# Kernel optimization log

Hardware: AMD Instinct MI355X
Metric: run time of the kernel (lower is better)

## Reference

```python
import jax, jax.numpy as jnp
import numpy as np

DIM = 512
HEADS = 8
EPS = 1e-3  # keras LayerNormalization default epsilon


def setup_inputs() -> dict:
    key = jax.random.key(0)
    ks = jax.random.split(key, 12)
    B, H, W, C = 8, 32, 32, DIM
    s = 0.02
    return {
        "x": jax.random.normal(ks[0], (B, H, W, C), jnp.float32),
        "ln_gamma": jnp.ones((C,), jnp.float32),
        "ln_beta": jnp.zeros((C,), jnp.float32),
        "qkv_d_w": jax.random.normal(ks[1], (C, 3 * C), jnp.float32) * s,
        "qkv_d_b": jnp.zeros((3 * C,), jnp.float32),
        "qkv_s_w": jax.random.normal(ks[2], (C, 3 * C), jnp.float32) * s,
        "qkv_s_b": jnp.zeros((3 * C,), jnp.float32),
        "proj_d_w": jax.random.normal(ks[3], (C, C), jnp.float32) * s,
        "proj_d_b": jnp.zeros((C,), jnp.float32),
        "proj_s_w": jax.random.normal(ks[4], (C, C), jnp.float32) * s,
        "proj_s_b": jnp.zeros((C,), jnp.float32),
        "fusion_weight": jnp.ones((2,), jnp.float32),
    }


def _split_heads(t, B, N):
    # [B, N, C] -> [B, heads, N, head_dim]
    return t.reshape(B, N, HEADS, -1).transpose(0, 2, 1, 3)


def _merge_heads(t, B, N, C):
    # [B, heads, N, head_dim] -> [B, N, C]
    return t.transpose(0, 2, 1, 3).reshape(B, N, C)


def reference(x, ln_gamma, ln_beta, qkv_d_w, qkv_d_b, qkv_s_w, qkv_s_b,
              proj_d_w, proj_d_b, proj_s_w, proj_s_b, fusion_weight):
    B, H, W, C = x.shape
    N = H * W
    scale = (C // HEADS) ** -0.5

    xf = x.reshape(B, N, C)
    mu = jnp.mean(xf, axis=-1, keepdims=True)
    var = jnp.var(xf, axis=-1, keepdims=True)
    xf = (xf - mu) * jax.lax.rsqrt(var + EPS) * ln_gamma + ln_beta

    # dense (softmax) branch
    qkv_d = xf @ qkv_d_w + qkv_d_b
    q_d, k_d, v_d = (
        _split_heads(t, B, N) for t in jnp.split(qkv_d, 3, axis=-1)
    )
    logits_d = jnp.einsum("bhnd,bhmd->bhnm", q_d, k_d) * scale
    out_d = jnp.einsum("bhnm,bhmd->bhnd", jax.nn.softmax(logits_d, axis=-1), v_d)
    out_d = _merge_heads(out_d, B, N, C) @ proj_d_w + proj_d_b

    # sparse (relu^2) branch
    qkv_s = xf @ qkv_s_w + qkv_s_b
    q_s, k_s, v_s = (
        _split_heads(t, B, N) for t in jnp.split(qkv_s, 3, axis=-1)
    )
    rq = jnp.square(jax.nn.relu(q_s))
    rk = jnp.square(jax.nn.relu(k_s))
    logits_s = jnp.einsum("bhnd,bhmd->bhnm", rq, rk) * scale
    out_s = jnp.einsum("bhnm,bhmd->bhnd", logits_s, v_s)
    out_s = _merge_heads(out_s, B, N, C) @ proj_s_w + proj_s_b

    alpha = jax.nn.softmax(fusion_weight)
    out = alpha[0] * out_s + alpha[1] * out_d
    return out.reshape(B, H, W, C)
```

## Files before the change

kernel.cpp:

```cpp
#include <hip/hip_runtime.h>
#include <math.h>

#define M_ROWS   8192
#define CDIM     512
#define QKV_N    1536
#define NTOK     1024
#define HEADS    8
#define HD       64
#define EPS      1e-3f
#define SCALE    0.125f
#define SCL2E    0.18033688011112042f

typedef __attribute__((ext_vector_type(8))) short short8;
typedef __attribute__((ext_vector_type(4))) float f32x4;
typedef unsigned short ushort_t;


__device__ __forceinline__ ushort_t f2bf(float f) {
    union { float f; unsigned int u; } v; v.f = f;
    unsigned int r = v.u + 0x7fffu + ((v.u >> 16) & 1u);
    return (ushort_t)(r >> 16);
}
__device__ __forceinline__ float bf2f(ushort_t u) {
    union { unsigned int u; float f; } v; v.u = ((unsigned int)u) << 16;
    return v.f;
}

__device__ __forceinline__ void get_alpha(const float* __restrict__ fw,
                                          float& a0, float& a1)
{
    const float m  = fmaxf(fw[0], fw[1]);
    const float e0 = __expf(fw[0] - m);
    const float e1 = __expf(fw[1] - m);
    const float inv = 1.0f / (e0 + e1);
    a0 = e0 * inv;
    a1 = e1 * inv;
}


__global__ __launch_bounds__(256) void ln_kernel(const float* __restrict__ x,
                                                 const float* __restrict__ gamma,
                                                 const float* __restrict__ beta,
                                                 ushort_t* __restrict__ xhi,
                                                 ushort_t* __restrict__ xlo)
{
    const int row = blockIdx.x;
    const int t   = threadIdx.x;
    const float2 v = ((const float2*)(x + (size_t)row * CDIM))[t];
    float s  = v.x + v.y;
    float ss = v.x * v.x + v.y * v.y;
#pragma unroll
    for (int off = 32; off > 0; off >>= 1) {
        s  += __shfl_xor(s,  off, 64);
        ss += __shfl_xor(ss, off, 64);
    }
    __shared__ float red[8];
    __shared__ float stats[2];
    const int wid = t >> 6, lane = t & 63;
    if (lane == 0) { red[wid] = s; red[4 + wid] = ss; }
    __syncthreads();
    if (t == 0) {
        const float S  = red[0] + red[1] + red[2] + red[3];
        const float SS = red[4] + red[5] + red[6] + red[7];
        const float mu  = S * (1.0f / CDIM);
        const float var = SS * (1.0f / CDIM) - mu * mu;
        stats[0] = mu;
        stats[1] = rsqrtf(var + EPS);
    }
    __syncthreads();
    const float mu = stats[0], rs = stats[1];
    const float2 gv = ((const float2*)gamma)[t];
    const float2 bv = ((const float2*)beta)[t];
    const float ox = (v.x - mu) * rs * gv.x + bv.x;
    const float oy = (v.y - mu) * rs * gv.y + bv.y;
    ushort2 h2, l2;
    h2.x = f2bf(ox); l2.x = f2bf(ox - bf2f(h2.x));
    h2.y = f2bf(oy); l2.y = f2bf(oy - bf2f(h2.y));
    ((ushort2*)(xhi + (size_t)row * CDIM))[t] = h2;
    ((ushort2*)(xlo + (size_t)row * CDIM))[t] = l2;
}


__global__ __launch_bounds__(256) void tconv_kernel(const float* __restrict__ W,
                                                    ushort_t* __restrict__ hiT,
                                                    ushort_t* __restrict__ loT,
                                                    int N, int ors, int coff)
{
    const int t  = threadIdx.x;
    const int bk = blockIdx.x * 64, bn = blockIdx.y * 64;
    __shared__ float tile[64][65];
#pragma unroll
    for (int i = 0; i < 4; ++i) {
        const int idx = t + i * 256;
        const int kl = idx >> 4, nl = (idx & 15) * 4;
        const float4 v = *(const float4*)(W + (size_t)(bk + kl) * N + bn + nl);
        tile[kl][nl] = v.x; tile[kl][nl + 1] = v.y;
        tile[kl][nl + 2] = v.z; tile[kl][nl + 3] = v.w;
    }
    __syncthreads();
#pragma unroll
    for (int i = 0; i < 2; ++i) {
        const int idx = t + i * 256;
        const int nl = idx >> 3, kc = (idx & 7) * 8;
        short8 hv, lv;
#pragma unroll
        for (int j = 0; j < 8; ++j) {
            const float f = tile[kc + j][nl];
            const ushort_t h = f2bf(f);
            hv[j] = (short)h;
            lv[j] = (short)f2bf(f - bf2f(h));
        }
        const size_t ob = (size_t)(bn + nl) * ors + coff + bk + kc;
        *(short8*)(hiT + ob) = hv;
        if (loT) *(short8*)(loT + ob) = lv;
    }
}


template<int MODE, int OUTBF>
__global__ __launch_bounds__(256) void gemm_bf16_mfma(const ushort_t* __restrict__ Ahi,
                                                      const ushort_t* __restrict__ Alo,
                                                      const ushort_t* __restrict__ Bhi,
                                                      const ushort_t* __restrict__ Blo,
                                                      const float* __restrict__ bias,
                                                      float* __restrict__ C,
                                                      ushort_t* __restrict__ Cb,
                                                      int N, int K)
{
    const int t  = threadIdx.x;
    const int l  = t & 63, w = t >> 6;
    const int wr = w >> 1, wc = w & 1;
    const int lr = l & 15, lg = l >> 4;
    const int bm = blockIdx.x * 128, bn = blockIdx.y * 128;

    __shared__ ushort_t As[MODE ? 2 : 1][128 * 64];
    __shared__ ushort_t Bs[MODE ? 2 : 1][128 * 64];

    f32x4 acc[4][4];
#pragma unroll
    for (int i = 0; i < 4; ++i)
#pragma unroll
        for (int j = 0; j < 4; ++j) acc[i][j] = (f32x4){0.f, 0.f, 0.f, 0.f};

    const int srow0  = t >> 3;
    const int schunk = t & 7;

    for (int kt = 0; kt < K; kt += 64) {
        __syncthreads();
#pragma unroll
        for (int i = 0; i < 4; ++i) {
            const int row = srow0 + i * 32;
            const int cs  = ((schunk ^ (row & 7)) * 8);
            const size_t ga = (size_t)(bm + row) * K + kt + schunk * 8;
            const size_t gb = (size_t)(bn + row) * K + kt + schunk * 8;
            *(short8*)(&As[0][row * 64 + cs]) = *(const short8*)(Ahi + ga);
            *(short8*)(&Bs[0][row * 64 + cs]) = *(const short8*)(Bhi + gb);
            if (MODE) {
                *(short8*)(&As[MODE ? 1 : 0][row * 64 + cs]) = *(const short8*)(Alo + ga);
                *(short8*)(&Bs[MODE ? 1 : 0][row * 64 + cs]) = *(const short8*)(Blo + gb);
            }
        }
        __syncthreads();
#pragma unroll
        for (int ks = 0; ks < 2; ++ks) {
            short8 ah[4], bh[4], al[4], bl[4];
#pragma unroll
            for (int mf = 0; mf < 4; ++mf) {
                const int row = wr * 64 + mf * 16 + lr;
                const int cs  = (((ks * 4 + lg) ^ (row & 7)) * 8);
                ah[mf] = *(const short8*)(&As[0][row * 64 + cs]);
                if (MODE) al[mf] = *(const short8*)(&As[MODE ? 1 : 0][row * 64 + cs]);
            }
#pragma unroll
            for (int nf = 0; nf < 4; ++nf) {
                const int row = wc * 64 + nf * 16 + lr;
                const int cs  = (((ks * 4 + lg) ^ (row & 7)) * 8);
                bh[nf] = *(const short8*)(&Bs[0][row * 64 + cs]);
                if (MODE) bl[nf] = *(const short8*)(&Bs[MODE ? 1 : 0][row * 64 + cs]);
            }
#pragma unroll
            for (int mf = 0; mf < 4; ++mf)
#pragma unroll
                for (int nf = 0; nf < 4; ++nf) {
                    acc[mf][nf] = __builtin_amdgcn_mfma_f32_16x16x32_bf16(ah[mf], bh[nf], acc[mf][nf], 0, 0, 0);
                    if (MODE) {
                        acc[mf][nf] = __builtin_amdgcn_mfma_f32_16x16x32_bf16(al[mf], bh[nf], acc[mf][nf], 0, 0, 0);
                        acc[mf][nf] = __builtin_amdgcn_mfma_f32_16x16x32_bf16(ah[mf], bl[nf], acc[mf][nf], 0, 0, 0);
                    }
                }
        }
    }
    float bv[4];
#pragma unroll
    for (int nf = 0; nf < 4; ++nf) bv[nf] = bias[bn + wc * 64 + nf * 16 + lr];
#pragma unroll
    for (int mf = 0; mf < 4; ++mf)
#pragma unroll
        for (int r = 0; r < 4; ++r) {
            const int row = bm + wr * 64 + mf * 16 + lg * 4 + r;
            if (OUTBF) {
                ushort_t* cp = Cb + (size_t)row * N + bn + wc * 64;
#pragma unroll
                for (int nf = 0; nf < 4; ++nf)
                    cp[nf * 16 + lr] = f2bf(acc[mf][nf][r] + bv[nf]);
            } else {
                float* cp = C + (size_t)row * N + bn + wc * 64;
#pragma unroll
                for (int nf = 0; nf < 4; ++nf)
                    cp[nf * 16 + lr] = acc[mf][nf][r] + bv[nf];
            }
        }
}


__global__ __launch_bounds__(256) void gemm_proj(const ushort_t* __restrict__ Ahi,
                                                 const ushort_t* __restrict__ Alo,
                                                 const ushort_t* __restrict__ Bhi,
                                                 const ushort_t* __restrict__ Blo,
                                                 const float* __restrict__ bias,
                                                 float* __restrict__ C)
{
    const int t  = threadIdx.x;
    const int l  = t & 63, w = t >> 6;
    const int wr = w >> 1, wc = w & 1;
    const int lr = l & 15, lg = l >> 4;
    const int bm = blockIdx.x * 64, bn = blockIdx.y * 128;

    __shared__ ushort_t As[2][64 * 64];
    __shared__ ushort_t Bs[2][128 * 64];

    f32x4 acc[2][4];
#pragma unroll
    for (int i = 0; i < 2; ++i)
#pragma unroll
        for (int j = 0; j < 4; ++j) acc[i][j] = (f32x4){0.f, 0.f, 0.f, 0.f};

    const int srow0  = t >> 3;
    const int schunk = t & 7;

    for (int kt = 0; kt < 512; kt += 64) {
        __syncthreads();
#pragma unroll
        for (int i = 0; i < 2; ++i) {
            const int row = srow0 + i * 32;
            const int cs  = ((schunk ^ (row & 7)) * 8);
            const size_t ga = (size_t)(bm + row) * 1024 + kt + schunk * 8;
            *(short8*)(&As[0][row * 64 + cs]) = *(const short8*)(Ahi + ga);
            *(short8*)(&As[1][row * 64 + cs]) = *(const short8*)(Alo + ga);
        }
#pragma unroll
        for (int i = 0; i < 4; ++i) {
            const int row = srow0 + i * 32;
            const int cs  = ((schunk ^ (row & 7)) * 8);
            const size_t gb = (size_t)(bn + row) * 1024 + kt + schunk * 8;
            *(short8*)(&Bs[0][row * 64 + cs]) = *(const short8*)(Bhi + gb);
            *(short8*)(&Bs[1][row * 64 + cs]) = *(const short8*)(Blo + gb);
        }
        __syncthreads();
#pragma unroll
        for (int ks = 0; ks < 2; ++ks) {
            short8 ah[2], al[2], bh[4], bl[4];
#pragma unroll
            for (int mf = 0; mf < 2; ++mf) {
                const int row = wr * 32 + mf * 16 + lr;
                const int cs  = (((ks * 4 + lg) ^ (row & 7)) * 8);
                ah[mf] = *(const short8*)(&As[0][row * 64 + cs]);
                al[mf] = *(const short8*)(&As[1][row * 64 + cs]);
            }
#pragma unroll
            for (int nf = 0; nf < 4; ++nf) {
                const int row = wc * 64 + nf * 16 + lr;
                const int cs  = (((ks * 4 + lg) ^ (row & 7)) * 8);
                bh[nf] = *(const short8*)(&Bs[0][row * 64 + cs]);
                bl[nf] = *(const short8*)(&Bs[1][row * 64 + cs]);
            }
#pragma unroll
            for (int mf = 0; mf < 2; ++mf)
#pragma unroll
                for (int nf = 0; nf < 4; ++nf) {
                    acc[mf][nf] = __builtin_amdgcn_mfma_f32_16x16x32_bf16(ah[mf], bh[nf], acc[mf][nf], 0, 0, 0);
                    acc[mf][nf] = __builtin_amdgcn_mfma_f32_16x16x32_bf16(al[mf], bh[nf], acc[mf][nf], 0, 0, 0);
                    acc[mf][nf] = __builtin_amdgcn_mfma_f32_16x16x32_bf16(ah[mf], bl[nf], acc[mf][nf], 0, 0, 0);
                }
        }
    }

    for (int kt = 512; kt < 1024; kt += 64) {
        __syncthreads();
#pragma unroll
        for (int i = 0; i < 2; ++i) {
            const int row = srow0 + i * 32;
            const int cs  = ((schunk ^ (row & 7)) * 8);
            const size_t ga = (size_t)(bm + row) * 1024 + kt + schunk * 8;
            *(short8*)(&As[0][row * 64 + cs]) = *(const short8*)(Ahi + ga);
        }
#pragma unroll
        for (int i = 0; i < 4; ++i) {
            const int row = srow0 + i * 32;
            const int cs  = ((schunk ^ (row & 7)) * 8);
            const size_t gb = (size_t)(bn + row) * 1024 + kt + schunk * 8;
            *(short8*)(&Bs[0][row * 64 + cs]) = *(const short8*)(Bhi + gb);
        }
        __syncthreads();
#pragma unroll
        for (int ks = 0; ks < 2; ++ks) {
            short8 ah[2], bh[4];
#pragma unroll
            for (int mf = 0; mf < 2; ++mf) {
                const int row = wr * 32 + mf * 16 + lr;
                const int cs  = (((ks * 4 + lg) ^ (row & 7)) * 8);
                ah[mf] = *(const short8*)(&As[0][row * 64 + cs]);
            }
#pragma unroll
            for (int nf = 0; nf < 4; ++nf) {
                const int row = wc * 64 + nf * 16 + lr;
                const int cs  = (((ks * 4 + lg) ^ (row & 7)) * 8);
                bh[nf] = *(const short8*)(&Bs[0][row * 64 + cs]);
            }
#pragma unroll
            for (int mf = 0; mf < 2; ++mf)
#pragma unroll
                for (int nf = 0; nf < 4; ++nf)
                    acc[mf][nf] = __builtin_amdgcn_mfma_f32_16x16x32_bf16(ah[mf], bh[nf], acc[mf][nf], 0, 0, 0);
        }
    }

    float bv[4];
#pragma unroll
    for (int nf = 0; nf < 4; ++nf) bv[nf] = bias[bn + wc * 64 + nf * 16 + lr];
#pragma unroll
    for (int mf = 0; mf < 2; ++mf)
#pragma unroll
        for (int r = 0; r < 4; ++r) {
            const int row = bm + wr * 32 + mf * 16 + lg * 4 + r;
            float* cp = C + (size_t)row * CDIM + bn + wc * 64;
#pragma unroll
            for (int nf = 0; nf < 4; ++nf)
                cp[nf * 16 + lr] = acc[mf][nf][r] + bv[nf];
        }
}


__global__ __launch_bounds__(256) void vt_kernel(const ushort_t* __restrict__ qkvd_bf,
                                                 ushort_t* __restrict__ vtg)
{
    const int t  = threadIdx.x;
    const int bh = blockIdx.x, nt = blockIdx.y;
    const int b  = bh >> 3, h = bh & 7;
    __shared__ ushort_t tile[64 * 72];
    const int row = t >> 2, c16 = (t & 3) * 16;
    const size_t src = (size_t)(b * NTOK + nt * 64 + row) * QKV_N + 2 * CDIM + h * HD + c16;
    *(short8*)(tile + row * 72 + c16)     = *(const short8*)(qkvd_bf + src);
    *(short8*)(tile + row * 72 + c16 + 8) = *(const short8*)(qkvd_bf + src + 8);
    __syncthreads();
    const int d = t >> 2, tc = (t & 3) * 16;
    short8 o0, o1;
#pragma unroll
    for (int i = 0; i < 8; ++i) {
        o0[i] = (short)tile[(tc + i) * 72 + d];
        o1[i] = (short)tile[(tc + 8 + i) * 72 + d];
    }
    const size_t dst = ((size_t)bh * 64 + d) * NTOK + nt * 64 + tc;
    *(short8*)(vtg + dst)     = o0;
    *(short8*)(vtg + dst + 8) = o1;
}


__global__ __launch_bounds__(256) void attn_dense_mfma(const ushort_t* __restrict__ qkvd_bf,
                                                       const ushort_t* __restrict__ vtg,
                                                       const float* __restrict__ fw,
                                                       ushort_t* __restrict__ athi)
{
    const int t  = threadIdx.x;
    const int l  = t & 63;
    const int w  = t >> 6;
    const int lr = l & 15;
    const int lg = l >> 4;

    const int blk = blockIdx.x;
    const int xcd = blk & 7;
    const int ixl = blk >> 3;
    const int bh  = ((ixl >> 4) << 3) + xcd;
    const int qt  = ixl & 15;
    const int b   = bh >> 3, h = bh & 7;

    __shared__ ushort_t Qs[64 * 72];
    __shared__ ushort_t Ks[64 * 72];
    __shared__ ushort_t Vs[64 * 72];
    __shared__ ushort_t Pq[64 * 72];

    const int srow = t >> 2, sc = (t & 3) * 16;

    {
        const size_t src = (size_t)(b * NTOK + qt * 64 + srow) * QKV_N + h * HD + sc;
        *(short8*)(Qs + srow * 72 + sc)     = *(const short8*)(qkvd_bf + src);
        *(short8*)(Qs + srow * 72 + sc + 8) = *(const short8*)(qkvd_bf + src + 8);
    }
    __syncthreads();

    const short8 bQ0 = *(const short8*)(Qs + (w * 16 + lr) * 72 + lg * 8);
    const short8 bQ1 = *(const short8*)(Qs + (w * 16 + lr) * 72 + 32 + lg * 8);

    f32x4 oacc[4];
#pragma unroll
    for (int i = 0; i < 4; ++i) oacc[i] = (f32x4){0.f, 0.f, 0.f, 0.f};
    float lsum = 0.f;

    for (int kt2 = 0; kt2 < 16; ++kt2) {
        __syncthreads();
        {
            const size_t ksrc = (size_t)(b * NTOK + kt2 * 64 + srow) * QKV_N + CDIM + h * HD + sc;
            *(short8*)(Ks + srow * 72 + sc)     = *(const short8*)(qkvd_bf + ksrc);
            *(short8*)(Ks + srow * 72 + sc + 8) = *(const short8*)(qkvd_bf + ksrc + 8);
            const size_t vsrc = ((size_t)bh * 64 + srow) * NTOK + kt2 * 64 + sc;
            *(short8*)(Vs + srow * 72 + sc)     = *(const short8*)(vtg + vsrc);
            *(short8*)(Vs + srow * 72 + sc + 8) = *(const short8*)(vtg + vsrc + 8);
        }
        __syncthreads();

#pragma unroll
        for (int kb = 0; kb < 4; ++kb) {
            const short8 aK0 = *(const short8*)(Ks + (kb * 16 + lr) * 72 + lg * 8);
            const short8 aK1 = *(const short8*)(Ks + (kb * 16 + lr) * 72 + 32 + lg * 8);
            f32x4 z = {0.f, 0.f, 0.f, 0.f};
            z = __builtin_amdgcn_mfma_f32_16x16x32_bf16(aK0, bQ0, z, 0, 0, 0);
            z = __builtin_amdgcn_mfma_f32_16x16x32_bf16(aK1, bQ1, z, 0, 0, 0);
            const float p0 = exp2f(z[0] * SCL2E);
            const float p1 = exp2f(z[1] * SCL2E);
            const float p2 = exp2f(z[2] * SCL2E);
            const float p3 = exp2f(z[3] * SCL2E);
            lsum += (p0 + p1) + (p2 + p3);
            unsigned int r01, r23;
            asm("v_cvt_pk_bf16_f32 %0, %1, %2" : "=v"(r01) : "v"(p0), "v"(p1));
            asm("v_cvt_pk_bf16_f32 %0, %1, %2" : "=v"(r23) : "v"(p2), "v"(p3));
            uint2 pw; pw.x = r01; pw.y = r23;
            *(uint2*)(Pq + (w * 16 + lr) * 72 + kb * 16 + lg * 4) = pw;
        }

        const short8 bP0 = *(const short8*)(Pq + (w * 16 + lr) * 72 + lg * 8);
        const short8 bP1 = *(const short8*)(Pq + (w * 16 + lr) * 72 + 32 + lg * 8);
#pragma unroll
        for (int nfd = 0; nfd < 4; ++nfd) {
            const short8 aV0 = *(const short8*)(Vs + (nfd * 16 + lr) * 72 + lg * 8);
            const short8 aV1 = *(const short8*)(Vs + (nfd * 16 + lr) * 72 + 32 + lg * 8);
            oacc[nfd] = __builtin_amdgcn_mfma_f32_16x16x32_bf16(aV0, bP0, oacc[nfd], 0, 0, 0);
            oacc[nfd] = __builtin_amdgcn_mfma_f32_16x16x32_bf16(aV1, bP1, oacc[nfd], 0, 0, 0);
        }
    }

    lsum += __shfl_xor(lsum, 16, 64);
    lsum += __shfl_xor(lsum, 32, 64);
    float a0, a1;
    get_alpha(fw, a0, a1);
    const float sc2 = a1 / lsum;
    const size_t orow = ((size_t)(b * NTOK + qt * 64 + w * 16 + lr)) * 1024 + CDIM + h * HD;
#pragma unroll
    for (int nfd = 0; nfd < 4; ++nfd) {
        ushort4 hw;
#pragma unroll
        for (int r = 0; r < 4; ++r)
            ((ushort_t*)&hw)[r] = f2bf(oacc[nfd][r] * sc2);
        *(ushort4*)(athi + orow + nfd * 16 + lg * 4) = hw;
    }
}


__global__ __launch_bounds__(256) void sparse_kv_kernel(const float* __restrict__ qkvs,
                                                        float* __restrict__ kvpart)
{
    const int t     = threadIdx.x;
    const int bh    = blockIdx.x >> 2;
    const int chunk = blockIdx.x & 3;
    const int b     = bh >> 3, h = bh & 7;
    const int j     = t >> 2, g = t & 3;
    __shared__ __align__(16) float ks[64 * 68];
    __shared__ __align__(16) float vs[64 * 68];
    float4 acc[4];
#pragma unroll
    for (int c4 = 0; c4 < 4; ++c4) acc[c4] = make_float4(0.f, 0.f, 0.f, 0.f);

    const size_t bbase = (size_t)b * NTOK * QKV_N;
    for (int mt = chunk * 4; mt < chunk * 4 + 4; ++mt) {
        __syncthreads();
        {
            const float* ksrc = qkvs + bbase + (size_t)(mt * 64) * QKV_N + CDIM + h * HD;
            const float* vsrc = ksrc + CDIM;
#pragma unroll
            for (int i = 0; i < 4; ++i) {
                const int idx = t + i * 256;
                const int row = idx >> 4, c4 = (idx & 15) * 4;
                *(float4*)(ks + row * 68 + c4) = *(const float4*)(ksrc + (size_t)row * QKV_N + c4);
                *(float4*)(vs + row * 68 + c4) = *(const float4*)(vsrc + (size_t)row * QKV_N + c4);
            }
        }
        __syncthreads();
#pragma unroll 4
        for (int m = 0; m < 64; ++m) {
            const float kkv = ks[m * 68 + j];
            const float rk  = fmaxf(kkv, 0.f);
            const float rk2 = rk * rk;
#pragma unroll
            for (int c4 = 0; c4 < 4; ++c4) {
                const float4 vv = *(const float4*)(vs + m * 68 + g * 16 + c4 * 4);
                acc[c4].x += rk2 * vv.x; acc[c4].y += rk2 * vv.y;
                acc[c4].z += rk2 * vv.z; acc[c4].w += rk2 * vv.w;
            }
        }
    }
#pragma unroll
    for (int c4 = 0; c4 < 4; ++c4) {
        float4 w = acc[c4];
        w.x *= SCALE; w.y *= SCALE; w.z *= SCALE; w.w *= SCALE;
        *(float4*)(kvpart + ((size_t)blockIdx.x << 12) + j * 64 + g * 16 + c4 * 4) = w;
    }
}


__global__ __launch_bounds__(256) void sparse_out_kernel(const float* __restrict__ qkvs,
                                                         const float* __restrict__ kvpart,
                                                         const float* __restrict__ fw,
                                                         ushort_t* __restrict__ athi,
                                                         ushort_t* __restrict__ atlo)
{
    const int t   = threadIdx.x;
    const int blk = blockIdx.x;
    const int qt  = blk & 15;
    const int bh  = blk >> 4;
    const int b   = bh >> 3, h = bh & 7;
    const int r   = t >> 2, g = t & 3;
    __shared__ __align__(16) float qs[64 * 68];
    __shared__ __align__(16) float kvs[64 * 68];
    {
        const float* qsrc = qkvs + (size_t)b * NTOK * QKV_N + (size_t)(qt * 64) * QKV_N + h * HD;
        const float* p0 = kvpart + ((size_t)(bh * 4) << 12);
#pragma unroll
        for (int i = 0; i < 4; ++i) {
            const int idx = t + i * 256;
            const int row = idx >> 4, c4 = (idx & 15) * 4;
            *(float4*)(qs + row * 68 + c4) = *(const float4*)(qsrc + (size_t)row * QKV_N + c4);
            const int o = row * 64 + c4;
            float4 s0 = *(const float4*)(p0 + o);
            const float4 s1 = *(const float4*)(p0 + 4096 + o);
            const float4 s2 = *(const float4*)(p0 + 8192 + o);
            const float4 s3 = *(const float4*)(p0 + 12288 + o);
            s0.x += s1.x + s2.x + s3.x; s0.y += s1.y + s2.y + s3.y;
            s0.z += s1.z + s2.z + s3.z; s0.w += s1.w + s2.w + s3.w;
            *(float4*)(kvs + row * 68 + c4) = s0;
        }
    }
    __syncthreads();
    float4 acc[4];
#pragma unroll
    for (int c4 = 0; c4 < 4; ++c4) acc[c4] = make_float4(0.f, 0.f, 0.f, 0.f);
#pragma unroll 4
    for (int jj = 0; jj < 64; ++jj) {
        const float qv  = qs[r * 68 + jj];
        const float rq  = fmaxf(qv, 0.f);
        const float rq2 = rq * rq;
#pragma unroll
        for (int c4 = 0; c4 < 4; ++c4) {
            const float4 kvv = *(const float4*)(kvs + jj * 68 + g * 16 + c4 * 4);
            acc[c4].x += rq2 * kvv.x; acc[c4].y += rq2 * kvv.y;
            acc[c4].z += rq2 * kvv.z; acc[c4].w += rq2 * kvv.w;
        }
    }
    float a0, a1;
    get_alpha(fw, a0, a1);
    const size_t orow = ((size_t)(b * NTOK + qt * 64 + r)) * 1024 + h * HD;
#pragma unroll
    for (int c4 = 0; c4 < 4; ++c4) {
        float4 w = acc[c4];
        w.x *= a0; w.y *= a0; w.z *= a0; w.w *= a0;
        ushort4 hw, lw;
        hw.x = f2bf(w.x); lw.x = f2bf(w.x - bf2f(hw.x));
        hw.y = f2bf(w.y); lw.y = f2bf(w.y - bf2f(hw.y));
        hw.z = f2bf(w.z); lw.z = f2bf(w.z - bf2f(hw.z));
        hw.w = f2bf(w.w); lw.w = f2bf(w.w - bf2f(hw.w));
        *(ushort4*)(athi + orow + g * 16 + c4 * 4) = hw;
        *(ushort4*)(atlo + orow + g * 16 + c4 * 4) = lw;
    }
}


__global__ void bias_comb_kernel(const float* __restrict__ bs,
                                 const float* __restrict__ bd,
                                 const float* __restrict__ fw,
                                 float* __restrict__ out)
{
    float a0, a1;
    get_alpha(fw, a0, a1);
    const int t = threadIdx.x;
    out[t] = a0 * bs[t] + a1 * bd[t];
}


extern "C" void kernel_launch(void* const* d_in, const int* in_sizes, int n_in,
                              void* d_out, int out_size, void* d_ws, size_t ws_size,
                              hipStream_t stream)
{
    (void)in_sizes; (void)n_in; (void)out_size; (void)ws_size;

    const float* x        = (const float*)d_in[0];
    const float* ln_g     = (const float*)d_in[1];
    const float* ln_b     = (const float*)d_in[2];
    const float* qkv_d_w  = (const float*)d_in[3];
    const float* qkv_d_b  = (const float*)d_in[4];
    const float* qkv_s_w  = (const float*)d_in[5];
    const float* qkv_s_b  = (const float*)d_in[6];
    const float* proj_d_w = (const float*)d_in[7];
    const float* proj_d_b = (const float*)d_in[8];
    const float* proj_s_w = (const float*)d_in[9];
    const float* proj_s_b = (const float*)d_in[10];
    const float* fw       = (const float*)d_in[11];

    float* ws = (float*)d_ws;
    float*    qkvs    = ws;
    float*    kvpart  = ws + (size_t)12582912;
    float*    biasc   = ws + (size_t)13631488;
    ushort_t* qkvd_bf = (ushort_t*)(ws + (size_t)14680064);
    ushort_t* vtg     = (ushort_t*)(ws + (size_t)20971520);
    ushort_t* athi    = (ushort_t*)(ws + (size_t)23068672);
    ushort_t* atlo    = (ushort_t*)(ws + (size_t)27262976);
    ushort_t* xhi     = (ushort_t*)(ws + (size_t)31457280);
    ushort_t* xlo     = (ushort_t*)(ws + (size_t)33554432);
    ushort_t* WdT_hi  = (ushort_t*)(ws + (size_t)35651584);
    ushort_t* WsT_hi  = (ushort_t*)(ws + (size_t)36044800);
    ushort_t* WsT_lo  = (ushort_t*)(ws + (size_t)36438016);
    ushort_t* WpT_hi  = (ushort_t*)(ws + (size_t)36831232);
    ushort_t* WpT_lo  = (ushort_t*)(ws + (size_t)37093376);

    ln_kernel<<<8192, 256, 0, stream>>>(x, ln_g, ln_b, xhi, xlo);
    tconv_kernel<<<dim3(8, 24), 256, 0, stream>>>(qkv_d_w, WdT_hi, nullptr, QKV_N, CDIM, 0);
    tconv_kernel<<<dim3(8, 24), 256, 0, stream>>>(qkv_s_w, WsT_hi, WsT_lo, QKV_N, CDIM, 0);
    tconv_kernel<<<dim3(8, 8), 256, 0, stream>>>(proj_s_w, WpT_hi, WpT_lo, CDIM, 1024, 0);
    tconv_kernel<<<dim3(8, 8), 256, 0, stream>>>(proj_d_w, WpT_hi, nullptr, CDIM, 1024, 512);
    bias_comb_kernel<<<1, 512, 0, stream>>>(proj_s_b, proj_d_b, fw, biasc);

    gemm_bf16_mfma<0, 1><<<dim3(64, 12), 256, 0, stream>>>(xhi, nullptr, WdT_hi, nullptr,
                                                           qkv_d_b, nullptr, qkvd_bf,
                                                           QKV_N, CDIM);
    gemm_bf16_mfma<1, 0><<<dim3(64, 12), 256, 0, stream>>>(xhi, xlo, WsT_hi, WsT_lo,
                                                           qkv_s_b, qkvs, nullptr,
                                                           QKV_N, CDIM);

    vt_kernel<<<dim3(64, 16), 256, 0, stream>>>(qkvd_bf, vtg);
    attn_dense_mfma<<<1024, 256, 0, stream>>>(qkvd_bf, vtg, fw, athi);

    sparse_kv_kernel<<<256, 256, 0, stream>>>(qkvs, kvpart);
    sparse_out_kernel<<<1024, 256, 0, stream>>>(qkvs, kvpart, fw, athi, atlo);

    gemm_proj<<<dim3(128, 4), 256, 0, stream>>>(athi, atlo, WpT_hi, WpT_lo,
                                                biasc, (float*)d_out);
}
```

Measured before the change: 198.6 us.

## Merge independent kernels into combined launches and add MFMA priority hints

Merges the layernorm, four weight-transpose conversions and the bias combine into one prep kernel that branches on block index. It likewise pairs the V-transpose with the sparse KV reduction, and the dense attention with the sparse output stage, so independent work shares a launch. This cuts launch count and the idle gaps between small kernels, and lets the two attention branches overlap on the GPU. It also wraps the attention MFMA sections in s_setprio. The cost is larger shared memory per block, since each merged kernel reserves the bigger branch's buffer, which may lower occupancy.

```diff
diff --git a/kernel.cpp b/kernel.cpp
--- a/kernel.cpp
+++ b/kernel.cpp
@@ -38,57 +38,13 @@
 }
 
 
-__global__ __launch_bounds__(256) void ln_kernel(const float* __restrict__ x,
-                                                 const float* __restrict__ gamma,
-                                                 const float* __restrict__ beta,
-                                                 ushort_t* __restrict__ xhi,
-                                                 ushort_t* __restrict__ xlo)
-{
-    const int row = blockIdx.x;
-    const int t   = threadIdx.x;
-    const float2 v = ((const float2*)(x + (size_t)row * CDIM))[t];
-    float s  = v.x + v.y;
-    float ss = v.x * v.x + v.y * v.y;
-#pragma unroll
-    for (int off = 32; off > 0; off >>= 1) {
-        s  += __shfl_xor(s,  off, 64);
-        ss += __shfl_xor(ss, off, 64);
-    }
-    __shared__ float red[8];
-    __shared__ float stats[2];
-    const int wid = t >> 6, lane = t & 63;
-    if (lane == 0) { red[wid] = s; red[4 + wid] = ss; }
-    __syncthreads();
-    if (t == 0) {
-        const float S  = red[0] + red[1] + red[2] + red[3];
-        const float SS = red[4] + red[5] + red[6] + red[7];
-        const float mu  = S * (1.0f / CDIM);
-        const float var = SS * (1.0f / CDIM) - mu * mu;
-        stats[0] = mu;
-        stats[1] = rsqrtf(var + EPS);
-    }
-    __syncthreads();
-    const float mu = stats[0], rs = stats[1];
-    const float2 gv = ((const float2*)gamma)[t];
-    const float2 bv = ((const float2*)beta)[t];
-    const float ox = (v.x - mu) * rs * gv.x + bv.x;
-    const float oy = (v.y - mu) * rs * gv.y + bv.y;
-    ushort2 h2, l2;
-    h2.x = f2bf(ox); l2.x = f2bf(ox - bf2f(h2.x));
-    h2.y = f2bf(oy); l2.y = f2bf(oy - bf2f(h2.y));
-    ((ushort2*)(xhi + (size_t)row * CDIM))[t] = h2;
-    ((ushort2*)(xlo + (size_t)row * CDIM))[t] = l2;
-}
-
-
-__global__ __launch_bounds__(256) void tconv_kernel(const float* __restrict__ W,
-                                                    ushort_t* __restrict__ hiT,
-                                                    ushort_t* __restrict__ loT,
-                                                    int N, int ors, int coff)
-{
-    const int t  = threadIdx.x;
-    const int bk = blockIdx.x * 64, bn = blockIdx.y * 64;
-    __shared__ float tile[64][65];
+__device__ __forceinline__ void tconv_body(const float* __restrict__ W,
+                                           ushort_t* __restrict__ hiT,
+                                           ushort_t* __restrict__ loT,
+                                           int N, int ors, int coff,
+                                           int bk, int bn, int t,
+                                           float (*tile)[65])
+{
 #pragma unroll
     for (int i = 0; i < 4; ++i) {
         const int idx = t + i * 256;
@@ -114,6 +70,95 @@
         *(short8*)(hiT + ob) = hv;
         if (loT) *(short8*)(loT + ob) = lv;
     }
+}
+
+__global__ __launch_bounds__(256) void prep_kernel(const float* __restrict__ x,
+                                                   const float* __restrict__ gamma,
+                                                   const float* __restrict__ beta,
+                                                   ushort_t* __restrict__ xhi,
+                                                   ushort_t* __restrict__ xlo,
+                                                   const float* __restrict__ qkv_d_w,
+                                                   ushort_t* __restrict__ WdT_hi,
+                                                   const float* __restrict__ qkv_s_w,
+                                                   ushort_t* __restrict__ WsT_hi,
+                                                   ushort_t* __restrict__ WsT_lo,
+                                                   const float* __restrict__ proj_s_w,
+                                                   const float* __restrict__ proj_d_w,
+                                                   ushort_t* __restrict__ WpT_hi,
+                                                   ushort_t* __restrict__ WpT_lo,
+                                                   const float* __restrict__ bs,
+                                                   const float* __restrict__ bd,
+                                                   const float* __restrict__ fw,
+                                                   float* __restrict__ biasc)
+{
+    __shared__ float tile[64][65];
+    __shared__ float red[8];
+    __shared__ float stats[2];
+    const int t = threadIdx.x;
+    const int blk = blockIdx.x;
+
+    if (blk < 8192) {
+        const int row = blk;
+        const float2 v = ((const float2*)(x + (size_t)row * CDIM))[t];
+        float s  = v.x + v.y;
+        float ss = v.x * v.x + v.y * v.y;
+#pragma unroll
+        for (int off = 32; off > 0; off >>= 1) {
+            s  += __shfl_xor(s,  off, 64);
+            ss += __shfl_xor(ss, off, 64);
+        }
+        const int wid = t >> 6, lane = t & 63;
+        if (lane == 0) { red[wid] = s; red[4 + wid] = ss; }
+        __syncthreads();
+        if (t == 0) {
+            const float S  = red[0] + red[1] + red[2] + red[3];
+            const float SS = red[4] + red[5] + red[6] + red[7];
+            const float mu  = S * (1.0f / CDIM);
+            const float var = SS * (1.0f / CDIM) - mu * mu;
+            stats[0] = mu;
+            stats[1] = rsqrtf(var + EPS);
+        }
+        __syncthreads();
+        const float mu = stats[0], rs = stats[1];
+        const float2 gv = ((const float2*)gamma)[t];
+        const float2 bv = ((const float2*)beta)[t];
+        const float ox = (v.x - mu) * rs * gv.x + bv.x;
+        const float oy = (v.y - mu) * rs * gv.y + bv.y;
+        ushort2 h2, l2;
+        h2.x = f2bf(ox); l2.x = f2bf(ox - bf2f(h2.x));
+        h2.y = f2bf(oy); l2.y = f2bf(oy - bf2f(h2.y));
+        ((ushort2*)(xhi + (size_t)row * CDIM))[t] = h2;
+        ((ushort2*)(xlo + (size_t)row * CDIM))[t] = l2;
+        return;
+    }
+    int idx = blk - 8192;
+    if (idx < 192) {
+        tconv_body(qkv_d_w, WdT_hi, nullptr, QKV_N, CDIM, 0,
+                   (idx & 7) * 64, (idx >> 3) * 64, t, tile);
+        return;
+    }
+    idx -= 192;
+    if (idx < 192) {
+        tconv_body(qkv_s_w, WsT_hi, WsT_lo, QKV_N, CDIM, 0,
+                   (idx & 7) * 64, (idx >> 3) * 64, t, tile);
+        return;
+    }
+    idx -= 192;
+    if (idx < 64) {
+        tconv_body(proj_s_w, WpT_hi, WpT_lo, CDIM, 1024, 0,
+                   (idx & 7) * 64, (idx >> 3) * 64, t, tile);
+        return;
+    }
+    idx -= 64;
+    if (idx < 64) {
+        tconv_body(proj_d_w, WpT_hi, nullptr, CDIM, 1024, 512,
+                   (idx & 7) * 64, (idx >> 3) * 64, t, tile);
+        return;
+    }
+    float a0, a1;
+    get_alpha(fw, a0, a1);
+    biasc[t]       = a0 * bs[t]       + a1 * bd[t];
+    biasc[t + 256] = a0 * bs[t + 256] + a1 * bd[t + 256];
 }
 
 
@@ -341,140 +386,43 @@
 }
 
 
-__global__ __launch_bounds__(256) void vt_kernel(const ushort_t* __restrict__ qkvd_bf,
-                                                 ushort_t* __restrict__ vtg)
-{
-    const int t  = threadIdx.x;
-    const int bh = blockIdx.x, nt = blockIdx.y;
-    const int b  = bh >> 3, h = bh & 7;
-    __shared__ ushort_t tile[64 * 72];
-    const int row = t >> 2, c16 = (t & 3) * 16;
-    const size_t src = (size_t)(b * NTOK + nt * 64 + row) * QKV_N + 2 * CDIM + h * HD + c16;
-    *(short8*)(tile + row * 72 + c16)     = *(const short8*)(qkvd_bf + src);
-    *(short8*)(tile + row * 72 + c16 + 8) = *(const short8*)(qkvd_bf + src + 8);
-    __syncthreads();
-    const int d = t >> 2, tc = (t & 3) * 16;
-    short8 o0, o1;
-#pragma unroll
-    for (int i = 0; i < 8; ++i) {
-        o0[i] = (short)tile[(tc + i) * 72 + d];
-        o1[i] = (short)tile[(tc + 8 + i) * 72 + d];
-    }
-    const size_t dst = ((size_t)bh * 64 + d) * NTOK + nt * 64 + tc;
-    *(short8*)(vtg + dst)     = o0;
-    *(short8*)(vtg + dst + 8) = o1;
-}
-
-
-__global__ __launch_bounds__(256) void attn_dense_mfma(const ushort_t* __restrict__ qkvd_bf,
-                                                       const ushort_t* __restrict__ vtg,
-                                                       const float* __restrict__ fw,
-                                                       ushort_t* __restrict__ athi)
-{
-    const int t  = threadIdx.x;
-    const int l  = t & 63;
-    const int w  = t >> 6;
-    const int lr = l & 15;
-    const int lg = l >> 4;
-
-    const int blk = blockIdx.x;
-    const int xcd = blk & 7;
-    const int ixl = blk >> 3;
-    const int bh  = ((ixl >> 4) << 3) + xcd;
-    const int qt  = ixl & 15;
-    const int b   = bh >> 3, h = bh & 7;
-
-    __shared__ ushort_t Qs[64 * 72];
-    __shared__ ushort_t Ks[64 * 72];
-    __shared__ ushort_t Vs[64 * 72];
-    __shared__ ushort_t Pq[64 * 72];
-
-    const int srow = t >> 2, sc = (t & 3) * 16;
-
-    {
-        const size_t src = (size_t)(b * NTOK + qt * 64 + srow) * QKV_N + h * HD + sc;
-        *(short8*)(Qs + srow * 72 + sc)     = *(const short8*)(qkvd_bf + src);
-        *(short8*)(Qs + srow * 72 + sc + 8) = *(const short8*)(qkvd_bf + src + 8);
-    }
-    __syncthreads();
-
-    const short8 bQ0 = *(const short8*)(Qs + (w * 16 + lr) * 72 + lg * 8);
-    const short8 bQ1 = *(const short8*)(Qs + (w * 16 + lr) * 72 + 32 + lg * 8);
-
-    f32x4 oacc[4];
-#pragma unroll
-    for (int i = 0; i < 4; ++i) oacc[i] = (f32x4){0.f, 0.f, 0.f, 0.f};
-    float lsum = 0.f;
-
-    for (int kt2 = 0; kt2 < 16; ++kt2) {
-        __syncthreads();
-        {
-            const size_t ksrc = (size_t)(b * NTOK + kt2 * 64 + srow) * QKV_N + CDIM + h * HD + sc;
-            *(short8*)(Ks + srow * 72 + sc)     = *(const short8*)(qkvd_bf + ksrc);
-            *(short8*)(Ks + srow * 72 + sc + 8) = *(const short8*)(qkvd_bf + ksrc + 8);
-            const size_t vsrc = ((size_t)bh * 64 + srow) * NTOK + kt2 * 64 + sc;
-            *(short8*)(Vs + srow * 72 + sc)     = *(const short8*)(vtg + vsrc);
-            *(short8*)(Vs + srow * 72 + sc + 8) = *(const short8*)(vtg + vsrc + 8);
-        }
-        __syncthreads();
-
-#pragma unroll
-        for (int kb = 0; kb < 4; ++kb) {
-            const short8 aK0 = *(const short8*)(Ks + (kb * 16 + lr) * 72 + lg * 8);
-            const short8 aK1 = *(const short8*)(Ks + (kb * 16 + lr) * 72 + 32 + lg * 8);
-            f32x4 z = {0.f, 0.f, 0.f, 0.f};
-            z = __builtin_amdgcn_mfma_f32_16x16x32_bf16(aK0, bQ0, z, 0, 0, 0);
-            z = __builtin_amdgcn_mfma_f32_16x16x32_bf16(aK1, bQ1, z, 0, 0, 0);
-            const float p0 = exp2f(z[0] * SCL2E);
-            const float p1 = exp2f(z[1] * SCL2E);
-            const float p2 = exp2f(z[2] * SCL2E);
-            const float p3 = exp2f(z[3] * SCL2E);
-            lsum += (p0 + p1) + (p2 + p3);
-            unsigned int r01, r23;
-            asm("v_cvt_pk_bf16_f32 %0, %1, %2" : "=v"(r01) : "v"(p0), "v"(p1));
-            asm("v_cvt_pk_bf16_f32 %0, %1, %2" : "=v"(r23) : "v"(p2), "v"(p3));
-            uint2 pw; pw.x = r01; pw.y = r23;
-            *(uint2*)(Pq + (w * 16 + lr) * 72 + kb * 16 + lg * 4) = pw;
-        }
-
-        const short8 bP0 = *(const short8*)(Pq + (w * 16 + lr) * 72 + lg * 8);
-        const short8 bP1 = *(const short8*)(Pq + (w * 16 + lr) * 72 + 32 + lg * 8);
-#pragma unroll
-        for (int nfd = 0; nfd < 4; ++nfd) {
-            const short8 aV0 = *(const short8*)(Vs + (nfd * 16 + lr) * 72 + lg * 8);
-            const short8 aV1 = *(const short8*)(Vs + (nfd * 16 + lr) * 72 + 32 + lg * 8);
-            oacc[nfd] = __builtin_amdgcn_mfma_f32_16x16x32_bf16(aV0, bP0, oacc[nfd], 0, 0, 0);
-            oacc[nfd] = __builtin_amdgcn_mfma_f32_16x16x32_bf16(aV1, bP1, oacc[nfd], 0, 0, 0);
-        }
-    }
-
-    lsum += __shfl_xor(lsum, 16, 64);
-    lsum += __shfl_xor(lsum, 32, 64);
-    float a0, a1;
-    get_alpha(fw, a0, a1);
-    const float sc2 = a1 / lsum;
-    const size_t orow = ((size_t)(b * NTOK + qt * 64 + w * 16 + lr)) * 1024 + CDIM + h * HD;
-#pragma unroll
-    for (int nfd = 0; nfd < 4; ++nfd) {
-        ushort4 hw;
-#pragma unroll
-        for (int r = 0; r < 4; ++r)
-            ((ushort_t*)&hw)[r] = f2bf(oacc[nfd][r] * sc2);
-        *(ushort4*)(athi + orow + nfd * 16 + lg * 4) = hw;
-    }
-}
-
-
-__global__ __launch_bounds__(256) void sparse_kv_kernel(const float* __restrict__ qkvs,
-                                                        float* __restrict__ kvpart)
-{
-    const int t     = threadIdx.x;
-    const int bh    = blockIdx.x >> 2;
-    const int chunk = blockIdx.x & 3;
+__global__ __launch_bounds__(256) void vt_skv_kernel(const ushort_t* __restrict__ qkvd_bf,
+                                                     ushort_t* __restrict__ vtg,
+                                                     const float* __restrict__ qkvs,
+                                                     float* __restrict__ kvpart)
+{
+    __shared__ __align__(16) float smem[8704];
+    const int t = threadIdx.x;
+
+    if (blockIdx.x < 1024) {
+        ushort_t* tile = (ushort_t*)smem;
+        const int bh = blockIdx.x & 63, nt = blockIdx.x >> 6;
+        const int b  = bh >> 3, h = bh & 7;
+        const int row = t >> 2, c16 = (t & 3) * 16;
+        const size_t src = (size_t)(b * NTOK + nt * 64 + row) * QKV_N + 2 * CDIM + h * HD + c16;
+        *(short8*)(tile + row * 72 + c16)     = *(const short8*)(qkvd_bf + src);
+        *(short8*)(tile + row * 72 + c16 + 8) = *(const short8*)(qkvd_bf + src + 8);
+        __syncthreads();
+        const int d = t >> 2, tc = (t & 3) * 16;
+        short8 o0, o1;
+#pragma unroll
+        for (int i = 0; i < 8; ++i) {
+            o0[i] = (short)tile[(tc + i) * 72 + d];
+            o1[i] = (short)tile[(tc + 8 + i) * 72 + d];
+        }
+        const size_t dst = ((size_t)bh * 64 + d) * NTOK + nt * 64 + tc;
+        *(short8*)(vtg + dst)     = o0;
+        *(short8*)(vtg + dst + 8) = o1;
+        return;
+    }
+
+    const int bid   = blockIdx.x - 1024;
+    const int bh    = bid >> 2;
+    const int chunk = bid & 3;
     const int b     = bh >> 3, h = bh & 7;
     const int j     = t >> 2, g = t & 3;
-    __shared__ __align__(16) float ks[64 * 68];
-    __shared__ __align__(16) float vs[64 * 68];
+    float* ks = smem;
+    float* vs = smem + 64 * 68;
     float4 acc[4];
 #pragma unroll
     for (int c4 = 0; c4 < 4; ++c4) acc[c4] = make_float4(0.f, 0.f, 0.f, 0.f);
@@ -511,25 +459,127 @@
     for (int c4 = 0; c4 < 4; ++c4) {
         float4 w = acc[c4];
         w.x *= SCALE; w.y *= SCALE; w.z *= SCALE; w.w *= SCALE;
-        *(float4*)(kvpart + ((size_t)blockIdx.x << 12) + j * 64 + g * 16 + c4 * 4) = w;
-    }
-}
-
-
-__global__ __launch_bounds__(256) void sparse_out_kernel(const float* __restrict__ qkvs,
-                                                         const float* __restrict__ kvpart,
-                                                         const float* __restrict__ fw,
-                                                         ushort_t* __restrict__ athi,
-                                                         ushort_t* __restrict__ atlo)
-{
-    const int t   = threadIdx.x;
-    const int blk = blockIdx.x;
+        *(float4*)(kvpart + ((size_t)bid << 12) + j * 64 + g * 16 + c4 * 4) = w;
+    }
+}
+
+
+__global__ __launch_bounds__(256) void attn_sout_kernel(const ushort_t* __restrict__ qkvd_bf,
+                                                        const ushort_t* __restrict__ vtg,
+                                                        const float* __restrict__ qkvs,
+                                                        const float* __restrict__ kvpart,
+                                                        const float* __restrict__ fw,
+                                                        ushort_t* __restrict__ athi,
+                                                        ushort_t* __restrict__ atlo)
+{
+    __shared__ __align__(16) float smem[9216];
+    const int t = threadIdx.x;
+
+    if (blockIdx.x < 1024) {
+        const int l  = t & 63;
+        const int w  = t >> 6;
+        const int lr = l & 15;
+        const int lg = l >> 4;
+
+        const int blk = blockIdx.x;
+        const int xcd = blk & 7;
+        const int ixl = blk >> 3;
+        const int bh  = ((ixl >> 4) << 3) + xcd;
+        const int qt  = ixl & 15;
+        const int b   = bh >> 3, h = bh & 7;
+
+        ushort_t* Qs = (ushort_t*)smem;
+        ushort_t* Ks = Qs + 64 * 72;
+        ushort_t* Vs = Ks + 64 * 72;
+        ushort_t* Pq = Vs + 64 * 72;
+
+        const int srow = t >> 2, sc = (t & 3) * 16;
+
+        {
+            const size_t src = (size_t)(b * NTOK + qt * 64 + srow) * QKV_N + h * HD + sc;
+            *(short8*)(Qs + srow * 72 + sc)     = *(const short8*)(qkvd_bf + src);
+            *(short8*)(Qs + srow * 72 + sc + 8) = *(const short8*)(qkvd_bf + src + 8);
+        }
+        __syncthreads();
+
+        const short8 bQ0 = *(const short8*)(Qs + (w * 16 + lr) * 72 + lg * 8);
+        const short8 bQ1 = *(const short8*)(Qs + (w * 16 + lr) * 72 + 32 + lg * 8);
+
+        f32x4 oacc[4];
+#pragma unroll
+        for (int i = 0; i < 4; ++i) oacc[i] = (f32x4){0.f, 0.f, 0.f, 0.f};
+        float lsum = 0.f;
+
+        for (int kt2 = 0; kt2 < 16; ++kt2) {
+            __syncthreads();
+            {
+                const size_t ksrc = (size_t)(b * NTOK + kt2 * 64 + srow) * QKV_N + CDIM + h * HD + sc;
+                *(short8*)(Ks + srow * 72 + sc)     = *(const short8*)(qkvd_bf + ksrc);
+                *(short8*)(Ks + srow * 72 + sc + 8) = *(const short8*)(qkvd_bf + ksrc + 8);
+                const size_t vsrc = ((size_t)bh * 64 + srow) * NTOK + kt2 * 64 + sc;
+                *(short8*)(Vs + srow * 72 + sc)     = *(const short8*)(vtg + vsrc);
+                *(short8*)(Vs + srow * 72 + sc + 8) = *(const short8*)(vtg + vsrc + 8);
+            }
+            __syncthreads();
+
+#pragma unroll
+            for (int kb = 0; kb < 4; ++kb) {
+                const short8 aK0 = *(const short8*)(Ks + (kb * 16 + lr) * 72 + lg * 8);
+                const short8 aK1 = *(const short8*)(Ks + (kb * 16 + lr) * 72 + 32 + lg * 8);
+                f32x4 z = {0.f, 0.f, 0.f, 0.f};
+                __builtin_amdgcn_s_setprio(1);
+                z = __builtin_amdgcn_mfma_f32_16x16x32_bf16(aK0, bQ0, z, 0, 0, 0);
+                z = __builtin_amdgcn_mfma_f32_16x16x32_bf16(aK1, bQ1, z, 0, 0, 0);
+                __builtin_amdgcn_s_setprio(0);
+                const float p0 = exp2f(z[0] * SCL2E);
+                const float p1 = exp2f(z[1] * SCL2E);
+                const float p2 = exp2f(z[2] * SCL2E);
+                const float p3 = exp2f(z[3] * SCL2E);
+                lsum += (p0 + p1) + (p2 + p3);
+                unsigned int r01, r23;
+                asm("v_cvt_pk_bf16_f32 %0, %1, %2" : "=v"(r01) : "v"(p0), "v"(p1));
+                asm("v_cvt_pk_bf16_f32 %0, %1, %2" : "=v"(r23) : "v"(p2), "v"(p3));
+                uint2 pw; pw.x = r01; pw.y = r23;
+                *(uint2*)(Pq + (w * 16 + lr) * 72 + kb * 16 + lg * 4) = pw;
+            }
+
+            const short8 bP0 = *(const short8*)(Pq + (w * 16 + lr) * 72 + lg * 8);
+            const short8 bP1 = *(const short8*)(Pq + (w * 16 + lr) * 72 + 32 + lg * 8);
+            __builtin_amdgcn_s_setprio(1);
+#pragma unroll
+            for (int nfd = 0; nfd < 4; ++nfd) {
+                const short8 aV0 = *(const short8*)(Vs + (nfd * 16 + lr) * 72 + lg * 8);
+                const short8 aV1 = *(const short8*)(Vs + (nfd * 16 + lr) * 72 + 32 + lg * 8);
+                oacc[nfd] = __builtin_amdgcn_mfma_f32_16x16x32_bf16(aV0, bP0, oacc[nfd], 0, 0, 0);
+                oacc[nfd] = __builtin_amdgcn_mfma_f32_16x16x32_bf16(aV1, bP1, oacc[nfd], 0, 0, 0);
+            }
+            __builtin_amdgcn_s_setprio(0);
+        }
+
+        lsum += __shfl_xor(lsum, 16, 64);
+        lsum += __shfl_xor(lsum, 32, 64);
+        float a0, a1;
+        get_alpha(fw, a0, a1);
+        const float sc2 = a1 / lsum;
+        const size_t orow = ((size_t)(b * NTOK + qt * 64 + w * 16 + lr)) * 1024 + CDIM + h * HD;
+#pragma unroll
+        for (int nfd = 0; nfd < 4; ++nfd) {
+            ushort4 hw;
+#pragma unroll
+            for (int r = 0; r < 4; ++r)
+                ((ushort_t*)&hw)[r] = f2bf(oacc[nfd][r] * sc2);
+            *(ushort4*)(athi + orow + nfd * 16 + lg * 4) = hw;
+        }
+        return;
+    }
+
+    const int blk = blockIdx.x - 1024;
     const int qt  = blk & 15;
     const int bh  = blk >> 4;
     const int b   = bh >> 3, h = bh & 7;
     const int r   = t >> 2, g = t & 3;
-    __shared__ __align__(16) float qs[64 * 68];
-    __shared__ __align__(16) float kvs[64 * 68];
+    float* qs  = smem;
+    float* kvs = smem + 64 * 68;
     {
         const float* qsrc = qkvs + (size_t)b * NTOK * QKV_N + (size_t)(qt * 64) * QKV_N + h * HD;
         const float* p0 = kvpart + ((size_t)(bh * 4) << 12);
@@ -579,18 +629,6 @@
         *(ushort4*)(athi + orow + g * 16 + c4 * 4) = hw;
         *(ushort4*)(atlo + orow + g * 16 + c4 * 4) = lw;
     }
-}
-
-
-__global__ void bias_comb_kernel(const float* __restrict__ bs,
-                                 const float* __restrict__ bd,
-                                 const float* __restrict__ fw,
-                                 float* __restrict__ out)
-{
-    float a0, a1;
-    get_alpha(fw, a0, a1);
-    const int t = threadIdx.x;
-    out[t] = a0 * bs[t] + a1 * bd[t];
 }
 
 
@@ -629,12 +667,11 @@
     ushort_t* WpT_hi  = (ushort_t*)(ws + (size_t)36831232);
     ushort_t* WpT_lo  = (ushort_t*)(ws + (size_t)37093376);
 
-    ln_kernel<<<8192, 256, 0, stream>>>(x, ln_g, ln_b, xhi, xlo);
-    tconv_kernel<<<dim3(8, 24), 256, 0, stream>>>(qkv_d_w, WdT_hi, nullptr, QKV_N, CDIM, 0);
-    tconv_kernel<<<dim3(8, 24), 256, 0, stream>>>(qkv_s_w, WsT_hi, WsT_lo, QKV_N, CDIM, 0);
-    tconv_kernel<<<dim3(8, 8), 256, 0, stream>>>(proj_s_w, WpT_hi, WpT_lo, CDIM, 1024, 0);
-    tconv_kernel<<<dim3(8, 8), 256, 0, stream>>>(proj_d_w, WpT_hi, nullptr, CDIM, 1024, 512);
-    bias_comb_kernel<<<1, 512, 0, stream>>>(proj_s_b, proj_d_b, fw, biasc);
+    prep_kernel<<<8705, 256, 0, stream>>>(x, ln_g, ln_b, xhi, xlo,
+                                          qkv_d_w, WdT_hi,
+                                          qkv_s_w, WsT_hi, WsT_lo,
+                                          proj_s_w, proj_d_w, WpT_hi, WpT_lo,
+                                          proj_s_b, proj_d_b, fw, biasc);
 
     gemm_bf16_mfma<0, 1><<<dim3(64, 12), 256, 0, stream>>>(xhi, nullptr, WdT_hi, nullptr,
                                                            qkv_d_b, nullptr, qkvd_bf,
@@ -643,11 +680,8 @@
                                                            qkv_s_b, qkvs, nullptr,
                                                            QKV_N, CDIM);
 
-    vt_kernel<<<dim3(64, 16), 256, 0, stream>>>(qkvd_bf, vtg);
-    attn_dense_mfma<<<1024, 256, 0, stream>>>(qkvd_bf, vtg, fw, athi);
-
-    sparse_kv_kernel<<<256, 256, 0, stream>>>(qkvs, kvpart);
-    sparse_out_kernel<<<1024, 256, 0, stream>>>(qkvs, kvpart, fw, athi, atlo);
+    vt_skv_kernel<<<1280, 256, 0, stream>>>(qkvd_bf, vtg, qkvs, kvpart);
+    attn_sout_kernel<<<2048, 256, 0, stream>>>(qkvd_bf, vtg, qkvs, kvpart, fw, athi, atlo);
 
     gemm_proj<<<dim3(128, 4), 256, 0, stream>>>(athi, atlo, WpT_hi, WpT_lo,
                                                 biasc, (float*)d_out);
```

Measured after the change: 183.9 us. 1.08x faster.
